# Kernel tuning notes

Measured on AMD Instinct MI355X. Metric: run time of the kernel, lower is better.

Reference implementation:

```python
import jax, jax.numpy as jnp
import numpy as np

B, H, W = 32, 64, 64
D = 8        # input_dim (capsule dim of incoming caps)
C = 8        # input_ch (number of incoming capsule types)
DIM = 8      # dim_capsule (output capsule dim)
NCH = 8      # n_channels (number of output capsule types)


def _gconv(x, w, groups, stride=1):
    # x: NHWC, w: HWIO with I = in_ch/groups, O = total out (grouped by output blocks)
    return jax.lax.conv_general_dilated(
        x, w, (stride, stride), 'SAME',
        dimension_numbers=('NHWC', 'HWIO', 'NHWC'),
        feature_group_count=groups)


def setup_inputs():
    key = jax.random.key(0)
    ks = jax.random.split(key, 5)
    inputs = jax.random.normal(ks[0], (B, H, W, D, C), jnp.float32)
    Att_W = jax.random.normal(ks[1], (1, 1, DIM, C, C * NCH), jnp.float32) * 0.05
    ConvTrans_W = jax.random.normal(ks[2], (3, 3, D, C * DIM * NCH), jnp.float32) * 0.05
    ConvTrans_B = jnp.zeros((C * DIM * NCH,), jnp.float32)
    FeaExt_W = jax.random.normal(ks[3], (3, 3, DIM, DIM * NCH), jnp.float32) * 0.05
    FeaExt_B = jnp.zeros((DIM * NCH,), jnp.float32)
    CapsAct_W = jax.random.normal(ks[4], (1, 1, DIM, DIM * NCH), jnp.float32) * 0.05
    CapsAct_B = jnp.zeros((DIM * NCH,), jnp.float32)
    return {'inputs': inputs, 'Att_W': Att_W, 'ConvTrans_W': ConvTrans_W,
            'ConvTrans_B': ConvTrans_B, 'FeaExt_W': FeaExt_W, 'FeaExt_B': FeaExt_B,
            'CapsAct_W': CapsAct_W, 'CapsAct_B': CapsAct_B}


def reference(inputs, Att_W, ConvTrans_W, ConvTrans_B, FeaExt_W, FeaExt_B,
              CapsAct_W, CapsAct_B):
    # --- ConvTrans: per input-capsule-type 3x3 conv (== grouped conv over C groups) ---
    # inputs [B,H,W,D,C] -> [B,H,W,C*D] with group-major ordering
    xt = jnp.transpose(inputs, (0, 1, 2, 4, 3)).reshape(B, H, W, C * D)
    # ConvTrans_W [3,3,D, C*DIM*NCH]: output block i is the kernel for input group i
    y = _gconv(xt, ConvTrans_W, groups=C) + ConvTrans_B  # [B,H,W, C*DIM*NCH]
    # -> u[b,h,w,d,c_in,n]  (matches concat+transpose in the original)
    u = y.reshape(B, H, W, C, DIM, NCH).transpose(0, 1, 2, 4, 3, 5)

    # --- Attention: conv3d with kernel [1,1,DIM,C,C] per output type n (VALID over DIM) ---
    # Att_W [1,1,DIM,C,C*NCH] -> A[d, c_in, n, c_out]
    A = Att_W[0, 0].reshape(DIM, C, NCH, C)
    att = jnp.einsum('bhwdcn,dcno->bhwon', u, A)       # [B,H,W,C,NCH]
    att = jax.nn.softmax(att, axis=3)                  # softmax over input_ch
    v = jnp.einsum('bhwdon,bhwon->bhwdn', u, att)      # weighted sum over input_ch

    # --- FeaExt (3x3, grouped over NCH) + ReLU, then CapsAct (1x1, grouped) ---
    vt = jnp.transpose(v, (0, 1, 2, 4, 3)).reshape(B, H, W, NCH * DIM)
    h1 = jax.nn.relu(_gconv(vt, FeaExt_W, groups=NCH) + FeaExt_B)
    h2 = _gconv(h1, CapsAct_W, groups=NCH) + CapsAct_B
    out = h2.reshape(B, H, W, NCH, DIM).transpose(0, 1, 2, 4, 3)  # [B,H,W,DIM,NCH]
    return out
```

## Files before the change

### kernel.cpp

```cpp
#include <hip/hip_runtime.h>

#define HH 64
#define WW 64

typedef _Float16 f16;
typedef f16 f16x8 __attribute__((ext_vector_type(8)));
typedef f16 f16x4 __attribute__((ext_vector_type(4)));
typedef float f32x4 __attribute__((ext_vector_type(4)));

#define M1_H 0
#define BU_H 49152
#define BF_H 98304
#define BC_H 110592
#define VT_H 114688
#define PREP_N (64 + 114688)

__global__ __launch_bounds__(256) void prep_kernel(
    const float* __restrict__ attw, const float* __restrict__ ctw,
    const float* __restrict__ ctb, const float* __restrict__ few,
    const float* __restrict__ caw, float* __restrict__ ws) {
  int i = blockIdx.x * 256 + threadIdx.x;
  if (i >= PREP_N) return;
  f16* hb = (f16*)(ws + 64);
  if (i < 64) {
    int s = i >> 4, l15 = i & 15;
    int o = 2 * s + (l15 >> 3), n = l15 & 7;
    float acc = 0.f;
    for (int c = 0; c < 8; ++c)
      for (int d = 0; d < 8; ++d)
        acc += ctb[c * 64 + d * 8 + n] * attw[d * 512 + c * 64 + n * 8 + o];
    ws[i] = acc;
    return;
  }
  int z = i - 64;
  if (z < BU_H) {
    int j = z & 7, lane = (z >> 3) & 63, rest = z >> 9;
    int rs = rest % 12, c = rest / 12;
    int r = rs >> 2, s = rs & 3;
    int q = lane >> 4, l15 = lane & 15;
    int t = r * 4 + q;
    int o = 2 * s + (l15 >> 3), n = l15 & 7;
    float acc = 0.f;
    if (t < 9)
      for (int d = 0; d < 8; ++d)
        acc += ctw[(t * 8 + j) * 512 + c * 64 + d * 8 + n] *
               attw[d * 512 + c * 64 + n * 8 + o];
    hb[M1_H + z] = (f16)acc;
  } else if (z < BF_H) {
    int z2 = z - BU_H;
    int j = z2 & 7, lane = (z2 >> 3) & 63, rest = z2 >> 9;
    int rs = rest % 12, c = rest / 12;
    int r = rs >> 2, s = rs & 3;
    int q = lane >> 4, l15 = lane & 15;
    int t = r * 4 + q;
    int d = 2 * s + (l15 >> 3), n = l15 & 7;
    float v = (t < 9) ? ctw[(t * 8 + j) * 512 + c * 64 + d * 8 + n] : 0.f;
    hb[z] = (f16)v;
  } else if (z < BC_H) {
    int z2 = z - BF_H;
    int j = z2 & 7, lane = (z2 >> 3) & 63, rest = z2 >> 9;
    int r = rest % 3, g = rest / 3;
    int q = lane >> 4, l15 = lane & 15;
    int t = r * 4 + q;
    int d = 2 * (j & 3) + (j >> 2);
    float v = 0.f;
    if (t < 9 && ((l15 >> 3) == (g & 1)))
      v = few[(t * 8 + d) * 64 + g * 8 + (l15 & 7)];
    hb[z] = (f16)v;
  } else if (z < VT_H) {
    int z2 = z - BC_H;
    int j = z2 & 7, lane = (z2 >> 3) & 63, rest = z2 >> 9;
    int s = rest & 3, c2 = rest >> 2;
    int q = lane >> 4, l15 = lane & 15;
    int nk = c2 * 4 + q;
    int nc = 2 * s + (l15 >> 3);
    float v = (nk == nc) ? caw[j * 64 + nc * 8 + (l15 & 7)] : 0.f;
    hb[z] = (f16)v;
  }
}

__global__ __launch_bounds__(256, 2) void caps_stage1(
    const float* __restrict__ in, const float* __restrict__ ws,
    const float* __restrict__ ctb, f16* __restrict__ vt) {
  __shared__ f16 xt[181 * 72];
  __shared__ f16 attb[128 * 72];
  int bid = blockIdx.x;
  int b = bid >> 5, t5 = bid & 31;
  int ty = t5 >> 3, tx = t5 & 7;
  int tid = threadIdx.x;

  for (int i = tid; i < 181 * 8; i += 256) {
    int c = i & 7, hp = i >> 3;
    float xs[8] = {0.f, 0.f, 0.f, 0.f, 0.f, 0.f, 0.f, 0.f};
    if (hp < 180) {
      int hy = hp / 10, hx = hp - hy * 10;
      int gy = ty * 16 + hy - 1, gx = tx * 8 + hx - 1;
      if (gy >= 0 && gy < HH && gx >= 0 && gx < WW) {
        const float* src = in + (((b * HH + gy) * WW + gx) * 64 + c);
#pragma unroll
        for (int d = 0; d < 8; ++d) xs[d] = src[d * 8];
      }
    }
    f16x8 pk;
#pragma unroll
    for (int d = 0; d < 8; ++d) pk[d] = (f16)xs[d];
    *(f16x8*)&xt[hp * 72 + c * 8] = pk;
  }
  __syncthreads();

  int w = __builtin_amdgcn_readfirstlane(tid >> 6);
  int lane = tid & 63;
  int q = lane >> 4, l15 = lane & 15;
  int h = l15 >> 3, n = l15 & 7;

  int hpt[2][3];
#pragma unroll
  for (int i2 = 0; i2 < 2; ++i2) {
    int pyA = (2 * w + i2) * 2 + h;
    int pxA = l15 & 7;
#pragma unroll
    for (int r = 0; r < 3; ++r) {
      int t = r * 4 + q;
      int hp = 180;
      if (t < 9) {
        int ky = t / 3, kx = t - ky * 3;
        hp = (pyA + ky) * 10 + pxA + kx;
      }
      hpt[i2][r] = hp * 72;
    }
  }

  const f16x8* m1v = (const f16x8*)((const f16*)(ws + 64) + M1_H);
  const f16x8* buv = (const f16x8*)((const f16*)(ws + 64) + BU_H);
  const float* lb = ws;

  f32x4 L[2][4];
#pragma unroll
  for (int s = 0; s < 4; ++s) {
    float v0 = lb[s * 16 + l15];
    L[0][s] = (f32x4){v0, v0, v0, v0};
    L[1][s] = (f32x4){v0, v0, v0, v0};
  }
#pragma unroll 1
  for (int c = 0; c < 8; ++c) {
    f16x8 bm[12];
#pragma unroll
    for (int rs = 0; rs < 12; ++rs) bm[rs] = m1v[(c * 12 + rs) * 64 + lane];
    f16x8 a[2][3];
#pragma unroll
    for (int i2 = 0; i2 < 2; ++i2)
#pragma unroll
      for (int r = 0; r < 3; ++r)
        a[i2][r] = *(const f16x8*)&xt[hpt[i2][r] + c * 8];
#pragma unroll
    for (int i2 = 0; i2 < 2; ++i2)
#pragma unroll
      for (int s = 0; s < 4; ++s)
#pragma unroll
        for (int r = 0; r < 3; ++r)
          L[i2][s] = __builtin_amdgcn_mfma_f32_16x16x32_f16(
              a[i2][r], bm[r * 4 + s], L[i2][s], 0, 0, 0);
  }

#pragma unroll
  for (int i2 = 0; i2 < 2; ++i2) {
    int pbase = (2 * w + i2) * 16 + q * 4;
#pragma unroll
    for (int r = 0; r < 4; ++r) {
      float v0 = L[i2][0][r], v1 = L[i2][1][r], v2 = L[i2][2][r], v3 = L[i2][3][r];
      float pm = fmaxf(fmaxf(v0, v1), fmaxf(v2, v3));
      float m = fmaxf(pm, __shfl_xor(pm, 8));
      float e0 = __expf(v0 - m), e1 = __expf(v1 - m);
      float e2 = __expf(v2 - m), e3 = __expf(v3 - m);
      float ps = e0 + e1 + e2 + e3;
      float inv = 1.f / (ps + __shfl_xor(ps, 8));
      int ab = (pbase + r) * 72 + n * 8 + h;
      attb[ab + 0] = (f16)(e0 * inv);
      attb[ab + 2] = (f16)(e1 * inv);
      attb[ab + 4] = (f16)(e2 * inv);
      attb[ab + 6] = (f16)(e3 * inv);
    }
  }
  __syncthreads();

  f16x8 atp[2][4];
#pragma unroll
  for (int i2 = 0; i2 < 2; ++i2)
#pragma unroll
    for (int r = 0; r < 4; ++r)
      atp[i2][r] = *(const f16x8*)&attb[((2 * w + i2) * 16 + q * 4 + r) * 72 + n * 8];

  f32x4 V[2][4];
#pragma unroll
  for (int s = 0; s < 4; ++s) {
    V[0][s] = (f32x4){0.f, 0.f, 0.f, 0.f};
    V[1][s] = (f32x4){0.f, 0.f, 0.f, 0.f};
  }
#pragma unroll 1
  for (int c = 0; c < 8; ++c) {
    f16x8 bu[12];
#pragma unroll
    for (int rs = 0; rs < 12; ++rs) bu[rs] = buv[(c * 12 + rs) * 64 + lane];
    f16x8 a[2][3];
#pragma unroll
    for (int i2 = 0; i2 < 2; ++i2)
#pragma unroll
      for (int r = 0; r < 3; ++r)
        a[i2][r] = *(const f16x8*)&xt[hpt[i2][r] + c * 8];
    f32x4 U[2][4];
#pragma unroll
    for (int s = 0; s < 4; ++s) {
      float bv = ctb[c * 64 + s * 16 + l15];
      U[0][s] = (f32x4){bv, bv, bv, bv};
      U[1][s] = (f32x4){bv, bv, bv, bv};
    }
#pragma unroll
    for (int i2 = 0; i2 < 2; ++i2)
#pragma unroll
      for (int s = 0; s < 4; ++s)
#pragma unroll
        for (int r = 0; r < 3; ++r)
          U[i2][s] = __builtin_amdgcn_mfma_f32_16x16x32_f16(
              a[i2][r], bu[r * 4 + s], U[i2][s], 0, 0, 0);
#pragma unroll
    for (int i2 = 0; i2 < 2; ++i2)
#pragma unroll
      for (int r = 0; r < 4; ++r) {
        float af = (float)atp[i2][r][c];
#pragma unroll
        for (int s = 0; s < 4; ++s) V[i2][s][r] += U[i2][s][r] * af;
      }
  }

  __syncthreads();
  f16* vtmp = attb;
#pragma unroll
  for (int i2 = 0; i2 < 2; ++i2)
#pragma unroll
    for (int r = 0; r < 4; ++r) {
      int p = (2 * w + i2) * 16 + q * 4 + r;
      f16x4 st;
#pragma unroll
      for (int s = 0; s < 4; ++s) st[s] = (f16)V[i2][s][r];
      *(f16x4*)&vtmp[p * 72 + n * 8 + h * 4] = st;
    }
  __syncthreads();
  for (int idx = tid; idx < 1024; idx += 256) {
    int p = idx >> 3, q2 = idx & 7;
    float4 val = *(float4*)&vtmp[p * 72 + q2 * 8];
    int gy = ty * 16 + (p >> 3), gx = tx * 8 + (p & 7);
    ((float4*)(vt + ((b * HH + gy) * WW + gx) * 64))[q2] = val;
  }
}

__global__ __launch_bounds__(256, 2) void caps_stage2(
    const f16* __restrict__ vt, const float* __restrict__ ws,
    const float* __restrict__ fb, const float* __restrict__ cab,
    float* __restrict__ out) {
  __shared__ float smemf[8704];
  f16* vtile = (f16*)smemf;
  int bid = blockIdx.x;
  int b = bid >> 5, t5 = bid & 31;
  int ty = t5 >> 3, tx = t5 & 7;
  int tid = threadIdx.x;

  for (int i = tid; i < 181 * 8; i += 256) {
    int q2 = i & 7, hp = i >> 3;
    float4 val = make_float4(0.f, 0.f, 0.f, 0.f);
    if (hp < 180) {
      int hy = hp / 10, hx = hp - hy * 10;
      int gy = ty * 16 + hy - 1, gx = tx * 8 + hx - 1;
      if (gy >= 0 && gy < HH && gx >= 0 && gx < WW)
        val = ((const float4*)(vt + ((b * HH + gy) * WW + gx) * 64))[q2];
    }
    *(float4*)&vtile[hp * 72 + q2 * 8] = val;
  }
  __syncthreads();

  int w = __builtin_amdgcn_readfirstlane(tid >> 6);
  int lane = tid & 63;
  int q = lane >> 4, l15 = lane & 15;
  int h = l15 >> 3, j7 = l15 & 7;

  int hpt[2][3];
#pragma unroll
  for (int i2 = 0; i2 < 2; ++i2) {
    int pyA = (2 * w + i2) * 2 + h;
#pragma unroll
    for (int r = 0; r < 3; ++r) {
      int t = r * 4 + q;
      int hp = 180;
      if (t < 9) {
        int ky = t / 3, kx = t - ky * 3;
        hp = (pyA + ky) * 10 + j7 + kx;
      }
      hpt[i2][r] = hp * 72;
    }
  }

  const f16x8* bfv = (const f16x8*)((const f16*)(ws + 64) + BF_H);
  const f16x8* bcv = (const f16x8*)((const f16*)(ws + 64) + BC_H);

  f32x4 L[2][4];
#pragma unroll
  for (int s = 0; s < 4; ++s) {
    float bvv = fb[(2 * s + h) * 8 + j7];
    L[0][s] = (f32x4){bvv, bvv, bvv, bvv};
    L[1][s] = (f32x4){bvv, bvv, bvv, bvv};
  }
#pragma unroll
  for (int g = 0; g < 8; ++g) {
    int sg = g >> 1;
#pragma unroll
    for (int r = 0; r < 3; ++r) {
      f16x8 bf = bfv[(g * 3 + r) * 64 + lane];
#pragma unroll
      for (int i2 = 0; i2 < 2; ++i2) {
        f16x8 a = *(const f16x8*)&vtile[hpt[i2][r] + g * 8];
        L[i2][sg] = __builtin_amdgcn_mfma_f32_16x16x32_f16(a, bf, L[i2][sg], 0, 0, 0);
      }
    }
  }
#pragma unroll
  for (int i2 = 0; i2 < 2; ++i2)
#pragma unroll
    for (int s = 0; s < 4; ++s)
#pragma unroll
      for (int r = 0; r < 4; ++r) L[i2][s][r] = fmaxf(L[i2][s][r], 0.f);

  __syncthreads();
  f16* h1t = (f16*)smemf;
#pragma unroll
  for (int i2 = 0; i2 < 2; ++i2)
#pragma unroll
    for (int s = 0; s < 4; ++s)
#pragma unroll
      for (int r = 0; r < 4; ++r)
        h1t[((2 * w + i2) * 16 + q * 4 + r) * 72 + (2 * s + h) * 8 + j7] =
            (f16)L[i2][s][r];
  __syncthreads();

  f32x4 H[2][4];
#pragma unroll
  for (int s = 0; s < 4; ++s) {
    float bvv = cab[(2 * s + h) * 8 + j7];
    H[0][s] = (f32x4){bvv, bvv, bvv, bvv};
    H[1][s] = (f32x4){bvv, bvv, bvv, bvv};
  }
#pragma unroll
  for (int c2 = 0; c2 < 2; ++c2) {
    f16x8 a2[2];
#pragma unroll
    for (int i2 = 0; i2 < 2; ++i2)
      a2[i2] = *(const f16x8*)&h1t[((2 * w + i2) * 16 + l15) * 72 + c2 * 32 + q * 8];
#pragma unroll
    for (int s = 0; s < 4; ++s) {
      f16x8 bc = bcv[(c2 * 4 + s) * 64 + lane];
#pragma unroll
      for (int i2 = 0; i2 < 2; ++i2)
        H[i2][s] = __builtin_amdgcn_mfma_f32_16x16x32_f16(a2[i2], bc, H[i2][s], 0, 0, 0);
    }
  }

  __syncthreads();
  float* outbuf = smemf;
#pragma unroll
  for (int i2 = 0; i2 < 2; ++i2)
#pragma unroll
    for (int s = 0; s < 4; ++s)
#pragma unroll
      for (int r = 0; r < 4; ++r)
        outbuf[((2 * w + i2) * 16 + q * 4 + r) * 68 + j7 * 8 + 2 * s + h] =
            H[i2][s][r];
  __syncthreads();

  for (int idx = tid; idx < 2048; idx += 256) {
    int p = idx >> 4, q4 = idx & 15;
    float4 val = *(float4*)&outbuf[p * 68 + q4 * 4];
    int gy = ty * 16 + (p >> 3), gx = tx * 8 + (p & 7);
    *(float4*)(out + ((b * HH + gy) * WW + gx) * 64 + q4 * 4) = val;
  }
}

extern "C" void kernel_launch(void* const* d_in, const int* in_sizes, int n_in,
                              void* d_out, int out_size, void* d_ws, size_t ws_size,
                              hipStream_t stream) {
  const float* inputs = (const float*)d_in[0];
  const float* attw   = (const float*)d_in[1];
  const float* ctw    = (const float*)d_in[2];
  const float* ctb    = (const float*)d_in[3];
  const float* few    = (const float*)d_in[4];
  const float* fb     = (const float*)d_in[5];
  const float* caw    = (const float*)d_in[6];
  const float* cab    = (const float*)d_in[7];
  float* out = (float*)d_out;
  float* ws  = (float*)d_ws;
  f16* vt = (f16*)(ws + 64) + VT_H;

  prep_kernel<<<(PREP_N + 255) / 256, 256, 0, stream>>>(attw, ctw, ctb, few, caw, ws);
  caps_stage1<<<32 * 32, 256, 0, stream>>>(inputs, ws, ctb, vt);
  caps_stage2<<<32 * 32, 256, 0, stream>>>(vt, ws, fb, cab, out);
}
```

Baseline: 149.9 us.

## Cut LDS usage: keep softmax weights in registers, write output in halves

Result: slower. 155.1 us (+3.5%).

```diff
diff --git a/kernel.cpp b/kernel.cpp
--- a/kernel.cpp
+++ b/kernel.cpp
@@ -6,6 +6,7 @@
 typedef _Float16 f16;
 typedef f16 f16x8 __attribute__((ext_vector_type(8)));
 typedef f16 f16x4 __attribute__((ext_vector_type(4)));
+typedef f16 f16x2 __attribute__((ext_vector_type(2)));
 typedef float f32x4 __attribute__((ext_vector_type(4)));
 
 #define M1_H 0
@@ -14,6 +15,8 @@
 #define BC_H 110592
 #define VT_H 114688
 #define PREP_N (64 + 114688)
+
+union U2 { f16x2 v; int i; };
 
 __global__ __launch_bounds__(256) void prep_kernel(
     const float* __restrict__ attw, const float* __restrict__ ctw,
@@ -83,7 +86,6 @@
     const float* __restrict__ in, const float* __restrict__ ws,
     const float* __restrict__ ctb, f16* __restrict__ vt) {
   __shared__ f16 xt[181 * 72];
-  __shared__ f16 attb[128 * 72];
   int bid = blockIdx.x;
   int b = bid >> 5, t5 = bid & 31;
   int ty = t5 >> 3, tx = t5 & 7;
@@ -162,9 +164,9 @@
               a[i2][r], bm[r * 4 + s], L[i2][s], 0, 0, 0);
   }
 
-#pragma unroll
-  for (int i2 = 0; i2 < 2; ++i2) {
-    int pbase = (2 * w + i2) * 16 + q * 4;
+  f16x2 P[2][4][4];
+#pragma unroll
+  for (int i2 = 0; i2 < 2; ++i2)
 #pragma unroll
     for (int r = 0; r < 4; ++r) {
       float v0 = L[i2][0][r], v1 = L[i2][1][r], v2 = L[i2][2][r], v3 = L[i2][3][r];
@@ -174,21 +176,18 @@
       float e2 = __expf(v2 - m), e3 = __expf(v3 - m);
       float ps = e0 + e1 + e2 + e3;
       float inv = 1.f / (ps + __shfl_xor(ps, 8));
-      int ab = (pbase + r) * 72 + n * 8 + h;
-      attb[ab + 0] = (f16)(e0 * inv);
-      attb[ab + 2] = (f16)(e1 * inv);
-      attb[ab + 4] = (f16)(e2 * inv);
-      attb[ab + 6] = (f16)(e3 * inv);
-    }
-  }
-  __syncthreads();
-
-  f16x8 atp[2][4];
-#pragma unroll
-  for (int i2 = 0; i2 < 2; ++i2)
-#pragma unroll
-    for (int r = 0; r < 4; ++r)
-      atp[i2][r] = *(const f16x8*)&attb[((2 * w + i2) * 16 + q * 4 + r) * 72 + n * 8];
+      f16 o0 = (f16)(e0 * inv), o1 = (f16)(e1 * inv);
+      f16 o2 = (f16)(e2 * inv), o3 = (f16)(e3 * inv);
+      U2 p01, p23, r01, r23;
+      p01.v = (f16x2){o0, o1};
+      p23.v = (f16x2){o2, o3};
+      r01.i = __shfl_xor(p01.i, 8);
+      r23.i = __shfl_xor(p23.i, 8);
+      P[i2][r][0] = h ? (f16x2){r01.v[0], o0} : (f16x2){o0, r01.v[0]};
+      P[i2][r][1] = h ? (f16x2){r01.v[1], o1} : (f16x2){o1, r01.v[1]};
+      P[i2][r][2] = h ? (f16x2){r23.v[0], o2} : (f16x2){o2, r23.v[0]};
+      P[i2][r][3] = h ? (f16x2){r23.v[1], o3} : (f16x2){o3, r23.v[1]};
+    }
 
   f32x4 V[2][4];
 #pragma unroll
@@ -226,14 +225,14 @@
     for (int i2 = 0; i2 < 2; ++i2)
 #pragma unroll
       for (int r = 0; r < 4; ++r) {
-        float af = (float)atp[i2][r][c];
+        float af = (float)P[i2][r][c >> 1][c & 1];
 #pragma unroll
         for (int s = 0; s < 4; ++s) V[i2][s][r] += U[i2][s][r] * af;
       }
   }
 
   __syncthreads();
-  f16* vtmp = attb;
+  f16* vtmp = xt;
 #pragma unroll
   for (int i2 = 0; i2 < 2; ++i2)
 #pragma unroll
@@ -257,8 +256,8 @@
     const f16* __restrict__ vt, const float* __restrict__ ws,
     const float* __restrict__ fb, const float* __restrict__ cab,
     float* __restrict__ out) {
-  __shared__ float smemf[8704];
-  f16* vtile = (f16*)smemf;
+  __shared__ f16 smem[181 * 72];
+  f16* vtile = smem;
   int bid = blockIdx.x;
   int b = bid >> 5, t5 = bid & 31;
   int ty = t5 >> 3, tx = t5 & 7;
@@ -329,7 +328,7 @@
       for (int r = 0; r < 4; ++r) L[i2][s][r] = fmaxf(L[i2][s][r], 0.f);
 
   __syncthreads();
-  f16* h1t = (f16*)smemf;
+  f16* h1t = smem;
 #pragma unroll
   for (int i2 = 0; i2 < 2; ++i2)
 #pragma unroll
@@ -363,22 +362,29 @@
   }
 
   __syncthreads();
-  float* outbuf = smemf;
-#pragma unroll
-  for (int i2 = 0; i2 < 2; ++i2)
-#pragma unroll
-    for (int s = 0; s < 4; ++s)
-#pragma unroll
-      for (int r = 0; r < 4; ++r)
-        outbuf[((2 * w + i2) * 16 + q * 4 + r) * 68 + j7 * 8 + 2 * s + h] =
-            H[i2][s][r];
-  __syncthreads();
-
-  for (int idx = tid; idx < 2048; idx += 256) {
-    int p = idx >> 4, q4 = idx & 15;
-    float4 val = *(float4*)&outbuf[p * 68 + q4 * 4];
-    int gy = ty * 16 + (p >> 3), gx = tx * 8 + (p & 7);
-    *(float4*)(out + ((b * HH + gy) * WW + gx) * 64 + q4 * 4) = val;
+  float* outbuf = (float*)smem;
+#pragma unroll
+  for (int hh = 0; hh < 2; ++hh) {
+    if ((w >> 1) == hh) {
+#pragma unroll
+      for (int i2 = 0; i2 < 2; ++i2)
+#pragma unroll
+        for (int s = 0; s < 4; ++s)
+#pragma unroll
+          for (int r = 0; r < 4; ++r) {
+            int p = ((2 * w + i2) * 16 + q * 4 + r) - hh * 64;
+            outbuf[p * 68 + j7 * 8 + 2 * s + h] = H[i2][s][r];
+          }
+    }
+    __syncthreads();
+    for (int idx = tid; idx < 1024; idx += 256) {
+      int p = idx >> 4, q4 = idx & 15;
+      float4 val = *(float4*)&outbuf[p * 68 + q4 * 4];
+      int gp = hh * 64 + p;
+      int gy = ty * 16 + (gp >> 3), gx = tx * 8 + (gp & 7);
+      *(float4*)(out + ((b * HH + gy) * WW + gx) * 64 + q4 * 4) = val;
+    }
+    if (hh == 0) __syncthreads();
   }
 }
 
```
